# Kernel optimization log

Hardware: AMD Instinct MI355X
Metric: run time of the kernel (lower is better)

Reference implementation:

```python
import jax, jax.numpy as jnp
import numpy as np

N = 50000
E = 800000
D = 128
NCLASS = 10


def setup_inputs() -> dict:
    key = jax.random.key(0)
    ks = jax.random.split(key, 12)
    stdv = 1.0 / np.sqrt(D)
    inp = {
        "x": jax.random.normal(ks[0], (N, D), dtype=jnp.float32),
        "edge_src": jax.random.randint(ks[1], (E,), 0, N, dtype=jnp.int32),
        "edge_dst": jax.random.randint(ks[2], (E,), 0, N, dtype=jnp.int32),
        "edge_weight": jax.random.uniform(ks[3], (E,), dtype=jnp.float32),
        "W1": jax.random.uniform(ks[4], (D, D), jnp.float32, -stdv, stdv),
        "b1": jax.random.uniform(ks[5], (D,), jnp.float32, -stdv, stdv),
        "W2": jax.random.uniform(ks[6], (D, D), jnp.float32, -stdv, stdv),
        "b2": jax.random.uniform(ks[7], (D,), jnp.float32, -stdv, stdv),
        "W3": jax.random.uniform(ks[8], (D, D), jnp.float32, -stdv, stdv),
        "b3": jax.random.uniform(ks[9], (D,), jnp.float32, -stdv, stdv),
        "lin_W": jax.random.normal(ks[10], (NCLASS, 3 * D), dtype=jnp.float32) * 0.05,
        "lin_b": jax.random.normal(ks[11], (NCLASS,), dtype=jnp.float32) * 0.05,
    }
    return inp


def _gcn_layer(h, W, b, edge_src, edge_dst, edge_weight):
    # support = h @ W  (dense GEMM), then spmm(adj, support) as gather-scale-scatter
    support = h @ W                                   # [N, out]
    msgs = support[edge_src] * edge_weight[:, None]   # [E, out]
    agg = jax.ops.segment_sum(msgs, edge_dst, num_segments=h.shape[0])
    return agg + b


def reference(x, edge_src, edge_dst, edge_weight, W1, b1, W2, b2, W3, b3, lin_W, lin_b):
    x1 = jax.nn.relu(_gcn_layer(x, W1, b1, edge_src, edge_dst, edge_weight))
    o1 = jnp.max(x1, axis=0)
    x2 = jax.nn.relu(_gcn_layer(x1, W2, b2, edge_src, edge_dst, edge_weight))
    o2 = jnp.max(x2, axis=0)
    x3 = _gcn_layer(x2, W3, b3, edge_src, edge_dst, edge_weight)
    o3 = jnp.max(x3, axis=0)
    lin_in = jnp.concatenate([o1, o2, o3], axis=0)    # [3*D]
    logits = lin_W @ lin_in + lin_b                   # [nclass]
    return jax.nn.log_softmax(logits, axis=0)
```

## Files before the change

### kernel.cpp

```cpp
#include <hip/hip_runtime.h>
#include <hip/hip_bf16.h>
#include <math.h>

#define NN 50000
#define NPAD 50048
#define NE 800000
#define DD 128
#define NCLS 10
#define SCAN_BLOCK 1024
#define NTILES ((NN + 1 + SCAN_BLOCK - 1) / SCAN_BLOCK)

typedef short s16x8 __attribute__((ext_vector_type(8)));
typedef float f32x4 __attribute__((ext_vector_type(4)));

__device__ __forceinline__ unsigned short f2bf(float x) {
  __hip_bfloat16 h = __float2bfloat16(x);
  return __builtin_bit_cast(unsigned short, h);
}
__device__ __forceinline__ float bflo(unsigned int u) { return __uint_as_float(u << 16); }
__device__ __forceinline__ float bfhi(unsigned int u) { return __uint_as_float(u & 0xFFFF0000u); }

__device__ __forceinline__ unsigned int fkey(float f) {
  unsigned int u = __float_as_uint(f);
  return u ^ ((u & 0x80000000u) ? 0xFFFFFFFFu : 0x80000000u);
}
__device__ __forceinline__ float funkey(unsigned int k) {
  unsigned int u = (k & 0x80000000u) ? (k ^ 0x80000000u) : ~k;
  return __uint_as_float(u);
}

__global__ void k_count(const int* __restrict__ edst, int* __restrict__ offs) {
  int e = blockIdx.x * blockDim.x + threadIdx.x;
  if (e < NE) atomicAdd(&offs[edst[e] + 1], 1);
}

__global__ void k_scan_partial(const int* __restrict__ offs, int* __restrict__ bsum) {
  __shared__ int red[SCAN_BLOCK];
  int i = blockIdx.x * SCAN_BLOCK + threadIdx.x;
  red[threadIdx.x] = (i < NN + 1) ? offs[i] : 0;
  __syncthreads();
  for (int off = SCAN_BLOCK / 2; off > 0; off >>= 1) {
    if ((int)threadIdx.x < off) red[threadIdx.x] += red[threadIdx.x + off];
    __syncthreads();
  }
  if (threadIdx.x == 0) bsum[blockIdx.x] = red[0];
}

__global__ void k_scan_bsum(int* __restrict__ bsum) {
  if (threadIdx.x == 0) {
    int run = 0;
    for (int i = 0; i < NTILES; ++i) { int v = bsum[i]; bsum[i] = run; run += v; }
  }
}

__global__ void k_scan_final(int* __restrict__ offs, const int* __restrict__ bsum,
                             int* __restrict__ cursor) {
  __shared__ int tmp[SCAN_BLOCK];
  int i = blockIdx.x * SCAN_BLOCK + threadIdx.x;
  int v = (i < NN + 1) ? offs[i] : 0;
  tmp[threadIdx.x] = v;
  __syncthreads();
  for (int off = 1; off < SCAN_BLOCK; off <<= 1) {
    int t = ((int)threadIdx.x >= off) ? tmp[threadIdx.x - off] : 0;
    __syncthreads();
    tmp[threadIdx.x] += t;
    __syncthreads();
  }
  int incl = tmp[threadIdx.x] + bsum[blockIdx.x];
  if (i < NN + 1) {
    offs[i] = incl;
    if (i < NN) cursor[i] = incl;
  }
}

__global__ void k_fill(const int* __restrict__ esrc, const int* __restrict__ edst,
                       const float* __restrict__ ew, int* __restrict__ cursor,
                       int2* __restrict__ csr) {
  int e = blockIdx.x * blockDim.x + threadIdx.x;
  if (e < NE) {
    int d = edst[e];
    int p = atomicAdd(&cursor[d], 1);
    csr[p] = make_int2(esrc[e], __float_as_int(ew[e]));
  }
}

__global__ __launch_bounds__(256) void k_cvtW(const float* __restrict__ W1,
    const float* __restrict__ W2, const float* __restrict__ W3,
    unsigned short* __restrict__ WT1, unsigned short* __restrict__ WT2,
    unsigned short* __restrict__ WT3, unsigned int* __restrict__ omax) {
  int i = blockIdx.x * 256 + threadIdx.x;
  if (i < 3 * DD) omax[i] = 0u;
  if (i < DD * DD) {
    int k = i >> 7, c = i & 127;
    WT1[c * DD + k] = f2bf(W1[i]);
    WT2[c * DD + k] = f2bf(W2[i]);
    WT3[c * DD + k] = f2bf(W3[i]);
  }
}

template <int F32IN>
__global__ __launch_bounds__(256) void k_mm(const void* __restrict__ Hv,
                                            const unsigned short* __restrict__ Wt,
                                            unsigned short* __restrict__ S) {
  __shared__ unsigned short Hl[32 * DD];
  char* lb = (char*)Hl;
  const int wave = threadIdx.x >> 6, lane = threadIdx.x & 63;
  const int l15 = lane & 15, lk16 = (lane >> 4);
  const int r0 = blockIdx.x * 32;

#pragma unroll
  for (int j = 0; j < 2; ++j) {
    const int idx = threadIdx.x + j * 256;
    const int B = idx * 16;
    const int row = B >> 8;
    const int addr = B ^ ((row & 7) << 4);
    if (F32IN) {
      const float* H = (const float*)Hv;
      const int r = r0 + row;
      float4 a = make_float4(0.f, 0.f, 0.f, 0.f), b = a;
      if (r < NN) {
        const float* src = H + (size_t)r * DD + ((B & 255) >> 1);
        a = *(const float4*)src;
        b = *(const float4*)(src + 4);
      }
      uint4 pv;
      pv.x = (uint)f2bf(a.x) | ((uint)f2bf(a.y) << 16);
      pv.y = (uint)f2bf(a.z) | ((uint)f2bf(a.w) << 16);
      pv.z = (uint)f2bf(b.x) | ((uint)f2bf(b.y) << 16);
      pv.w = (uint)f2bf(b.z) | ((uint)f2bf(b.w) << 16);
      *(uint4*)(lb + addr) = pv;
    } else {
      const char* H = (const char*)Hv;
      uint4 v = *(const uint4*)(H + (size_t)r0 * 256 + B);
      *(uint4*)(lb + addr) = v;
    }
  }
  __syncthreads();

  const int cbase = wave * 32;
  s16x8 Af[2][4];
#pragma unroll
  for (int m = 0; m < 2; ++m)
#pragma unroll
    for (int ks = 0; ks < 4; ++ks)
      Af[m][ks] = *(const s16x8*)&Wt[(cbase + m * 16 + l15) * DD + ks * 32 + lk16 * 8];

  s16x8 Bf[2][4];
#pragma unroll
  for (int n = 0; n < 2; ++n) {
    const int row = n * 16 + l15;
#pragma unroll
    for (int ks = 0; ks < 4; ++ks) {
      const int B = row * 256 + ks * 64 + lk16 * 16;
      Bf[n][ks] = *(const s16x8*)(lb + (B ^ ((row & 7) << 4)));
    }
  }

  f32x4 acc[2][2];
#pragma unroll
  for (int m = 0; m < 2; ++m)
#pragma unroll
    for (int n = 0; n < 2; ++n) acc[m][n] = (f32x4){0.f, 0.f, 0.f, 0.f};

#pragma unroll
  for (int ks = 0; ks < 4; ++ks)
#pragma unroll
    for (int m = 0; m < 2; ++m)
#pragma unroll
      for (int n = 0; n < 2; ++n)
        acc[m][n] = __builtin_amdgcn_mfma_f32_16x16x32_bf16(Af[m][ks], Bf[n][ks],
                                                            acc[m][n], 0, 0, 0);

  __syncthreads();
#pragma unroll
  for (int m = 0; m < 2; ++m)
#pragma unroll
    for (int n = 0; n < 2; ++n) {
      const int row = n * 16 + l15;
      const int colb = (cbase + m * 16 + 4 * lk16) * 2;
      const int B = row * 256 + colb;
      uint2 pv;
      pv.x = (uint)f2bf(acc[m][n][0]) | ((uint)f2bf(acc[m][n][1]) << 16);
      pv.y = (uint)f2bf(acc[m][n][2]) | ((uint)f2bf(acc[m][n][3]) << 16);
      *(uint2*)(lb + (B ^ ((row & 7) << 4))) = pv;
    }
  __syncthreads();
#pragma unroll
  for (int j = 0; j < 2; ++j) {
    const int idx = threadIdx.x + j * 256;
    const int B = idx * 16;
    const int row = B >> 8;
    uint4 v = *(const uint4*)(lb + (B ^ ((row & 7) << 4)));
    *(uint4*)((char*)S + (size_t)r0 * 256 + B) = v;
  }
}

__device__ __forceinline__ void fma8(float* acc, float w, uint4 u) {
  acc[0] = fmaf(w, bflo(u.x), acc[0]);
  acc[1] = fmaf(w, bfhi(u.x), acc[1]);
  acc[2] = fmaf(w, bflo(u.y), acc[2]);
  acc[3] = fmaf(w, bfhi(u.y), acc[3]);
  acc[4] = fmaf(w, bflo(u.z), acc[4]);
  acc[5] = fmaf(w, bfhi(u.z), acc[5]);
  acc[6] = fmaf(w, bflo(u.w), acc[6]);
  acc[7] = fmaf(w, bfhi(u.w), acc[7]);
}

__global__ __launch_bounds__(256) void k_agg(const unsigned short* __restrict__ S,
                                             const int2* __restrict__ csr,
                                             const int* __restrict__ offs,
                                             const float* __restrict__ bias,
                                             unsigned short* __restrict__ Xout,
                                             unsigned int* __restrict__ omax,
                                             int do_relu) {
  __shared__ unsigned int cmax[DD];
  for (int i = threadIdx.x; i < DD; i += 256) cmax[i] = 0u;
  __syncthreads();
  const int lane = threadIdx.x & 63;
  const int wave = threadIdx.x >> 6;
  const int q = lane >> 4;
  const int t = lane & 15;
  const int gwave = blockIdx.x * 4 + wave;
  const int nwaves = gridDim.x * 4;
  const unsigned short* Scol = S + t * 8;

  float bcol[8];
  {
    float4 b0 = *(const float4*)&bias[t * 8];
    float4 b1 = *(const float4*)&bias[t * 8 + 4];
    bcol[0] = b0.x; bcol[1] = b0.y; bcol[2] = b0.z; bcol[3] = b0.w;
    bcol[4] = b1.x; bcol[5] = b1.y; bcol[6] = b1.z; bcol[7] = b1.w;
  }
  float mx[8];
#pragma unroll
  for (int j = 0; j < 8; ++j) mx[j] = -INFINITY;

  for (int d0 = gwave * 2; d0 < NN; d0 += nwaves * 2) {
    const int oA = offs[d0];
    const int oM = offs[d0 + 1];
    const int oE = offs[d0 + 2];
    int eA = oA + q; const int eA1 = oM;
    int eB = oM + q; const int eB1 = oE;
    float accA[8] = {0.f, 0.f, 0.f, 0.f, 0.f, 0.f, 0.f, 0.f};
    float accB[8] = {0.f, 0.f, 0.f, 0.f, 0.f, 0.f, 0.f, 0.f};

    while (__any((eA < eA1) || (eB < eB1))) {
      const bool pa0 = eA < eA1,      pa1 = eA + 4 < eA1;
      const bool pa2 = eA + 8 < eA1,  pa3 = eA + 12 < eA1;
      const bool pb0 = eB < eB1,      pb1 = eB + 4 < eB1;
      const bool pb2 = eB + 8 < eB1,  pb3 = eB + 12 < eB1;
      int2 a0, a1, a2, a3, b0, b1, b2, b3;
      if (pa0) a0 = csr[eA];
      if (pa1) a1 = csr[eA + 4];
      if (pa2) a2 = csr[eA + 8];
      if (pa3) a3 = csr[eA + 12];
      if (pb0) b0 = csr[eB];
      if (pb1) b1 = csr[eB + 4];
      if (pb2) b2 = csr[eB + 8];
      if (pb3) b3 = csr[eB + 12];
      uint4 uA0, uA1, uA2, uA3, uB0, uB1, uB2, uB3;
      if (pa0) uA0 = *(const uint4*)&Scol[(size_t)a0.x * DD];
      if (pa1) uA1 = *(const uint4*)&Scol[(size_t)a1.x * DD];
      if (pa2) uA2 = *(const uint4*)&Scol[(size_t)a2.x * DD];
      if (pa3) uA3 = *(const uint4*)&Scol[(size_t)a3.x * DD];
      if (pb0) uB0 = *(const uint4*)&Scol[(size_t)b0.x * DD];
      if (pb1) uB1 = *(const uint4*)&Scol[(size_t)b1.x * DD];
      if (pb2) uB2 = *(const uint4*)&Scol[(size_t)b2.x * DD];
      if (pb3) uB3 = *(const uint4*)&Scol[(size_t)b3.x * DD];
      if (pa0) fma8(accA, __int_as_float(a0.y), uA0);
      if (pa1) fma8(accA, __int_as_float(a1.y), uA1);
      if (pa2) fma8(accA, __int_as_float(a2.y), uA2);
      if (pa3) fma8(accA, __int_as_float(a3.y), uA3);
      if (pb0) fma8(accB, __int_as_float(b0.y), uB0);
      if (pb1) fma8(accB, __int_as_float(b1.y), uB1);
      if (pb2) fma8(accB, __int_as_float(b2.y), uB2);
      if (pb3) fma8(accB, __int_as_float(b3.y), uB3);
      eA += 16; eB += 16;
    }

#pragma unroll
    for (int j = 0; j < 8; ++j) {
      accA[j] += __shfl_xor(accA[j], 16, 64);
      accA[j] += __shfl_xor(accA[j], 32, 64);
      accA[j] += bcol[j];
      accB[j] += __shfl_xor(accB[j], 16, 64);
      accB[j] += __shfl_xor(accB[j], 32, 64);
      accB[j] += bcol[j];
      if (do_relu) {
        accA[j] = fmaxf(accA[j], 0.f);
        accB[j] = fmaxf(accB[j], 0.f);
      }
      mx[j] = fmaxf(mx[j], fmaxf(accA[j], accB[j]));
    }
    if (Xout) {
      if (q == 0) {
        uint4 xv;
        xv.x = (uint)f2bf(accA[0]) | ((uint)f2bf(accA[1]) << 16);
        xv.y = (uint)f2bf(accA[2]) | ((uint)f2bf(accA[3]) << 16);
        xv.z = (uint)f2bf(accA[4]) | ((uint)f2bf(accA[5]) << 16);
        xv.w = (uint)f2bf(accA[6]) | ((uint)f2bf(accA[7]) << 16);
        *(uint4*)&Xout[(size_t)d0 * DD + t * 8] = xv;
      } else if (q == 1) {
        uint4 xv;
        xv.x = (uint)f2bf(accB[0]) | ((uint)f2bf(accB[1]) << 16);
        xv.y = (uint)f2bf(accB[2]) | ((uint)f2bf(accB[3]) << 16);
        xv.z = (uint)f2bf(accB[4]) | ((uint)f2bf(accB[5]) << 16);
        xv.w = (uint)f2bf(accB[6]) | ((uint)f2bf(accB[7]) << 16);
        *(uint4*)&Xout[(size_t)(d0 + 1) * DD + t * 8] = xv;
      }
    }
  }
  if (q == 0) {
#pragma unroll
    for (int j = 0; j < 8; ++j) atomicMax(&cmax[t * 8 + j], fkey(mx[j]));
  }
  __syncthreads();
  for (int i = threadIdx.x; i < DD; i += 256) atomicMax(&omax[i], cmax[i]);
}

__global__ void k_head(const unsigned int* __restrict__ omax,
                       const float* __restrict__ linW,
                       const float* __restrict__ linb,
                       float* __restrict__ out) {
  __shared__ float o[3 * DD];
  __shared__ float logits[NCLS];
  int t = threadIdx.x;
  if (t < 3 * DD) o[t] = funkey(omax[t]);
  __syncthreads();
  if (t < NCLS) {
    float acc = linb[t];
    for (int j = 0; j < 3 * DD; ++j) acc = fmaf(linW[t * 3 * DD + j], o[j], acc);
    logits[t] = acc;
  }
  __syncthreads();
  if (t == 0) {
    float m = -INFINITY;
    for (int c = 0; c < NCLS; ++c) m = fmaxf(m, logits[c]);
    float s = 0.f;
    for (int c = 0; c < NCLS; ++c) s += expf(logits[c] - m);
    float ls = logf(s);
    for (int c = 0; c < NCLS; ++c) out[c] = logits[c] - m - ls;
  }
}

extern "C" void kernel_launch(void* const* d_in, const int* in_sizes, int n_in,
                              void* d_out, int out_size, void* d_ws, size_t ws_size,
                              hipStream_t stream) {
  const float* x    = (const float*)d_in[0];
  const int*   esrc = (const int*)d_in[1];
  const int*   edst = (const int*)d_in[2];
  const float* ew   = (const float*)d_in[3];
  const float* W1   = (const float*)d_in[4];
  const float* b1   = (const float*)d_in[5];
  const float* W2   = (const float*)d_in[6];
  const float* b2   = (const float*)d_in[7];
  const float* W3   = (const float*)d_in[8];
  const float* b3   = (const float*)d_in[9];
  const float* linW = (const float*)d_in[10];
  const float* linb = (const float*)d_in[11];
  float* out = (float*)d_out;

  size_t off = 0;
  auto alloc = [&](size_t bytes) {
    void* p = (char*)d_ws + off;
    off += (bytes + 255) & ~(size_t)255;
    return p;
  };
  unsigned short* X1   = (unsigned short*)alloc((size_t)NPAD * DD * 2);
  unsigned short* X2   = (unsigned short*)alloc((size_t)NPAD * DD * 2);
  unsigned short* S    = (unsigned short*)alloc((size_t)NPAD * DD * 2);
  unsigned short* WT1  = (unsigned short*)alloc((size_t)DD * DD * 2);
  unsigned short* WT2  = (unsigned short*)alloc((size_t)DD * DD * 2);
  unsigned short* WT3  = (unsigned short*)alloc((size_t)DD * DD * 2);
  int*          offs   = (int*)alloc((NN + 2) * 4);
  int*          cursor = (int*)alloc(NN * 4);
  int2*         csr    = (int2*)alloc((size_t)NE * 8);
  unsigned int* omax   = (unsigned int*)alloc(3 * DD * 4);
  int*          bsum   = (int*)alloc(NTILES * 4);
  (void)ws_size; (void)n_in; (void)in_sizes; (void)out_size;

  hipMemsetAsync(offs, 0, (NN + 2) * 4, stream);
  k_count<<<(NE + 255) / 256, 256, 0, stream>>>(edst, offs);
  k_scan_partial<<<NTILES, SCAN_BLOCK, 0, stream>>>(offs, bsum);
  k_scan_bsum<<<1, 64, 0, stream>>>(bsum);
  k_scan_final<<<NTILES, SCAN_BLOCK, 0, stream>>>(offs, bsum, cursor);
  k_fill<<<(NE + 255) / 256, 256, 0, stream>>>(esrc, edst, ew, cursor, csr);

  k_cvtW<<<(DD * DD + 255) / 256, 256, 0, stream>>>(W1, W2, W3, WT1, WT2, WT3, omax);

  const int mm_grid = NPAD / 32;
  k_mm<1><<<mm_grid, 256, 0, stream>>>(x, WT1, S);
  k_agg<<<2048, 256, 0, stream>>>(S, csr, offs, b1, X1, omax, 1);
  k_mm<0><<<mm_grid, 256, 0, stream>>>(X1, WT2, S);
  k_agg<<<2048, 256, 0, stream>>>(S, csr, offs, b2, X2, omax + DD, 1);
  k_mm<0><<<mm_grid, 256, 0, stream>>>(X2, WT3, S);
  k_agg<<<2048, 256, 0, stream>>>(S, csr, offs, b3, nullptr, omax + 2 * DD, 0);

  k_head<<<1, 384, 0, stream>>>(omax, linW, linb, out);
}
```

Measured before the change: 447.8 us.

## Split aggregation into column slices with XCD-aware block mapping and nontemporal loads

The aggregation kernel now gives each wave one destination node and only a 32-column slice of the feature row, instead of two nodes across all 128 columns. The slice is picked from blockIdx modulo 8, so blocks working on the same slice presumably land on the same XCD and share a smaller L2 working set. Each lane group now gathers 8 bytes per edge, and CSR reads and output writes use nontemporal hints. In exchange, the CSR edge list is read four times (once per slice), there are more gather instructions per byte, and the cross-lane reduction gains an extra shuffle stage.

New measurement: 461.4 us. +3.0%, slower.

```diff
diff --git a/kernel.cpp b/kernel.cpp
--- a/kernel.cpp
+++ b/kernel.cpp
@@ -195,127 +195,87 @@
   }
 }
 
-__device__ __forceinline__ void fma8(float* acc, float w, uint4 u) {
-  acc[0] = fmaf(w, bflo(u.x), acc[0]);
-  acc[1] = fmaf(w, bfhi(u.x), acc[1]);
-  acc[2] = fmaf(w, bflo(u.y), acc[2]);
-  acc[3] = fmaf(w, bfhi(u.y), acc[3]);
-  acc[4] = fmaf(w, bflo(u.z), acc[4]);
-  acc[5] = fmaf(w, bfhi(u.z), acc[5]);
-  acc[6] = fmaf(w, bflo(u.w), acc[6]);
-  acc[7] = fmaf(w, bfhi(u.w), acc[7]);
-}
-
 __global__ __launch_bounds__(256) void k_agg(const unsigned short* __restrict__ S,
-                                             const int2* __restrict__ csr,
+                                             const long* __restrict__ csr8,
                                              const int* __restrict__ offs,
                                              const float* __restrict__ bias,
                                              unsigned short* __restrict__ Xout,
                                              unsigned int* __restrict__ omax,
                                              int do_relu) {
-  __shared__ unsigned int cmax[DD];
-  for (int i = threadIdx.x; i < DD; i += 256) cmax[i] = 0u;
+  __shared__ unsigned int cmax[32];
+  if (threadIdx.x < 32) cmax[threadIdx.x] = 0u;
   __syncthreads();
   const int lane = threadIdx.x & 63;
   const int wave = threadIdx.x >> 6;
-  const int q = lane >> 4;
-  const int t = lane & 15;
-  const int gwave = blockIdx.x * 4 + wave;
-  const int nwaves = gridDim.x * 4;
-  const unsigned short* Scol = S + t * 8;
-
-  float bcol[8];
-  {
-    float4 b0 = *(const float4*)&bias[t * 8];
-    float4 b1 = *(const float4*)&bias[t * 8 + 4];
-    bcol[0] = b0.x; bcol[1] = b0.y; bcol[2] = b0.z; bcol[3] = b0.w;
-    bcol[4] = b1.x; bcol[5] = b1.y; bcol[6] = b1.z; bcol[7] = b1.w;
-  }
-  float mx[8];
-#pragma unroll
-  for (int j = 0; j < 8; ++j) mx[j] = -INFINITY;
-
-  for (int d0 = gwave * 2; d0 < NN; d0 += nwaves * 2) {
-    const int oA = offs[d0];
-    const int oM = offs[d0 + 1];
-    const int oE = offs[d0 + 2];
-    int eA = oA + q; const int eA1 = oM;
-    int eB = oM + q; const int eB1 = oE;
-    float accA[8] = {0.f, 0.f, 0.f, 0.f, 0.f, 0.f, 0.f, 0.f};
-    float accB[8] = {0.f, 0.f, 0.f, 0.f, 0.f, 0.f, 0.f, 0.f};
-
-    while (__any((eA < eA1) || (eB < eB1))) {
-      const bool pa0 = eA < eA1,      pa1 = eA + 4 < eA1;
-      const bool pa2 = eA + 8 < eA1,  pa3 = eA + 12 < eA1;
-      const bool pb0 = eB < eB1,      pb1 = eB + 4 < eB1;
-      const bool pb2 = eB + 8 < eB1,  pb3 = eB + 12 < eB1;
-      int2 a0, a1, a2, a3, b0, b1, b2, b3;
-      if (pa0) a0 = csr[eA];
-      if (pa1) a1 = csr[eA + 4];
-      if (pa2) a2 = csr[eA + 8];
-      if (pa3) a3 = csr[eA + 12];
-      if (pb0) b0 = csr[eB];
-      if (pb1) b1 = csr[eB + 4];
-      if (pb2) b2 = csr[eB + 8];
-      if (pb3) b3 = csr[eB + 12];
-      uint4 uA0, uA1, uA2, uA3, uB0, uB1, uB2, uB3;
-      if (pa0) uA0 = *(const uint4*)&Scol[(size_t)a0.x * DD];
-      if (pa1) uA1 = *(const uint4*)&Scol[(size_t)a1.x * DD];
-      if (pa2) uA2 = *(const uint4*)&Scol[(size_t)a2.x * DD];
-      if (pa3) uA3 = *(const uint4*)&Scol[(size_t)a3.x * DD];
-      if (pb0) uB0 = *(const uint4*)&Scol[(size_t)b0.x * DD];
-      if (pb1) uB1 = *(const uint4*)&Scol[(size_t)b1.x * DD];
-      if (pb2) uB2 = *(const uint4*)&Scol[(size_t)b2.x * DD];
-      if (pb3) uB3 = *(const uint4*)&Scol[(size_t)b3.x * DD];
-      if (pa0) fma8(accA, __int_as_float(a0.y), uA0);
-      if (pa1) fma8(accA, __int_as_float(a1.y), uA1);
-      if (pa2) fma8(accA, __int_as_float(a2.y), uA2);
-      if (pa3) fma8(accA, __int_as_float(a3.y), uA3);
-      if (pb0) fma8(accB, __int_as_float(b0.y), uB0);
-      if (pb1) fma8(accB, __int_as_float(b1.y), uB1);
-      if (pb2) fma8(accB, __int_as_float(b2.y), uB2);
-      if (pb3) fma8(accB, __int_as_float(b3.y), uB3);
-      eA += 16; eB += 16;
-    }
-
-#pragma unroll
-    for (int j = 0; j < 8; ++j) {
-      accA[j] += __shfl_xor(accA[j], 16, 64);
-      accA[j] += __shfl_xor(accA[j], 32, 64);
-      accA[j] += bcol[j];
-      accB[j] += __shfl_xor(accB[j], 16, 64);
-      accB[j] += __shfl_xor(accB[j], 32, 64);
-      accB[j] += bcol[j];
-      if (do_relu) {
-        accA[j] = fmaxf(accA[j], 0.f);
-        accB[j] = fmaxf(accB[j], 0.f);
+  const int g = lane >> 3;
+  const int t8 = lane & 7;
+  const int sgrp = blockIdx.x & 7;
+  const int slice = sgrp & 3;
+  const int half = sgrp >> 2;
+  const int bpg = (int)gridDim.x >> 3;
+  const int wsl = (half * bpg + (blockIdx.x >> 3)) * 4 + wave;
+  const int nstride = bpg * 8;
+  const int c0 = slice * 32 + t8 * 4;
+  const unsigned short* Sc = S + c0;
+
+  const float4 b4 = *(const float4*)&bias[c0];
+  float mx0 = -INFINITY, mx1 = -INFINITY, mx2 = -INFINITY, mx3 = -INFINITY;
+
+  for (int d = wsl; d < NN; d += nstride) {
+    const int e1 = offs[d + 1];
+    int e = offs[d] + g;
+    float a0 = 0.f, a1 = 0.f, a2 = 0.f, a3 = 0.f;
+    while (__any(e < e1)) {
+      const bool p0 = e < e1, p1 = e + 8 < e1;
+      long ce0 = 0, ce1 = 0;
+      if (p0) ce0 = __builtin_nontemporal_load(&csr8[e]);
+      if (p1) ce1 = __builtin_nontemporal_load(&csr8[e + 8]);
+      uint2 u0, u1;
+      if (p0) u0 = *(const uint2*)&Sc[(size_t)(int)ce0 * DD];
+      if (p1) u1 = *(const uint2*)&Sc[(size_t)(int)ce1 * DD];
+      if (p0) {
+        const float w = __uint_as_float((unsigned int)((unsigned long)ce0 >> 32));
+        a0 = fmaf(w, bflo(u0.x), a0);
+        a1 = fmaf(w, bfhi(u0.x), a1);
+        a2 = fmaf(w, bflo(u0.y), a2);
+        a3 = fmaf(w, bfhi(u0.y), a3);
       }
-      mx[j] = fmaxf(mx[j], fmaxf(accA[j], accB[j]));
-    }
-    if (Xout) {
-      if (q == 0) {
-        uint4 xv;
-        xv.x = (uint)f2bf(accA[0]) | ((uint)f2bf(accA[1]) << 16);
-        xv.y = (uint)f2bf(accA[2]) | ((uint)f2bf(accA[3]) << 16);
-        xv.z = (uint)f2bf(accA[4]) | ((uint)f2bf(accA[5]) << 16);
-        xv.w = (uint)f2bf(accA[6]) | ((uint)f2bf(accA[7]) << 16);
-        *(uint4*)&Xout[(size_t)d0 * DD + t * 8] = xv;
-      } else if (q == 1) {
-        uint4 xv;
-        xv.x = (uint)f2bf(accB[0]) | ((uint)f2bf(accB[1]) << 16);
-        xv.y = (uint)f2bf(accB[2]) | ((uint)f2bf(accB[3]) << 16);
-        xv.z = (uint)f2bf(accB[4]) | ((uint)f2bf(accB[5]) << 16);
-        xv.w = (uint)f2bf(accB[6]) | ((uint)f2bf(accB[7]) << 16);
-        *(uint4*)&Xout[(size_t)(d0 + 1) * DD + t * 8] = xv;
+      if (p1) {
+        const float w = __uint_as_float((unsigned int)((unsigned long)ce1 >> 32));
+        a0 = fmaf(w, bflo(u1.x), a0);
+        a1 = fmaf(w, bfhi(u1.x), a1);
+        a2 = fmaf(w, bflo(u1.y), a2);
+        a3 = fmaf(w, bfhi(u1.y), a3);
       }
-    }
-  }
-  if (q == 0) {
-#pragma unroll
-    for (int j = 0; j < 8; ++j) atomicMax(&cmax[t * 8 + j], fkey(mx[j]));
-  }
-  __syncthreads();
-  for (int i = threadIdx.x; i < DD; i += 256) atomicMax(&omax[i], cmax[i]);
+      e += 16;
+    }
+    a0 += __shfl_xor(a0, 8, 64);  a1 += __shfl_xor(a1, 8, 64);
+    a2 += __shfl_xor(a2, 8, 64);  a3 += __shfl_xor(a3, 8, 64);
+    a0 += __shfl_xor(a0, 16, 64); a1 += __shfl_xor(a1, 16, 64);
+    a2 += __shfl_xor(a2, 16, 64); a3 += __shfl_xor(a3, 16, 64);
+    a0 += __shfl_xor(a0, 32, 64); a1 += __shfl_xor(a1, 32, 64);
+    a2 += __shfl_xor(a2, 32, 64); a3 += __shfl_xor(a3, 32, 64);
+    a0 += b4.x; a1 += b4.y; a2 += b4.z; a3 += b4.w;
+    if (do_relu) {
+      a0 = fmaxf(a0, 0.f); a1 = fmaxf(a1, 0.f);
+      a2 = fmaxf(a2, 0.f); a3 = fmaxf(a3, 0.f);
+    }
+    mx0 = fmaxf(mx0, a0); mx1 = fmaxf(mx1, a1);
+    mx2 = fmaxf(mx2, a2); mx3 = fmaxf(mx3, a3);
+    if (Xout && g == 0) {
+      unsigned long lv = (unsigned long)((unsigned int)f2bf(a0) | ((unsigned int)f2bf(a1) << 16))
+                       | ((unsigned long)((unsigned int)f2bf(a2) | ((unsigned int)f2bf(a3) << 16)) << 32);
+      __builtin_nontemporal_store((long)lv, (long*)&Xout[(size_t)d * DD + c0]);
+    }
+  }
+  if (g == 0) {
+    atomicMax(&cmax[t8 * 4 + 0], fkey(mx0));
+    atomicMax(&cmax[t8 * 4 + 1], fkey(mx1));
+    atomicMax(&cmax[t8 * 4 + 2], fkey(mx2));
+    atomicMax(&cmax[t8 * 4 + 3], fkey(mx3));
+  }
+  __syncthreads();
+  if (threadIdx.x < 32) atomicMax(&omax[slice * 32 + threadIdx.x], cmax[threadIdx.x]);
 }
 
 __global__ void k_head(const unsigned int* __restrict__ omax,
@@ -389,12 +349,13 @@
   k_cvtW<<<(DD * DD + 255) / 256, 256, 0, stream>>>(W1, W2, W3, WT1, WT2, WT3, omax);
 
   const int mm_grid = NPAD / 32;
+  const long* csr8 = (const long*)csr;
   k_mm<1><<<mm_grid, 256, 0, stream>>>(x, WT1, S);
-  k_agg<<<2048, 256, 0, stream>>>(S, csr, offs, b1, X1, omax, 1);
+  k_agg<<<2048, 256, 0, stream>>>(S, csr8, offs, b1, X1, omax, 1);
   k_mm<0><<<mm_grid, 256, 0, stream>>>(X1, WT2, S);
-  k_agg<<<2048, 256, 0, stream>>>(S, csr, offs, b2, X2, omax + DD, 1);
+  k_agg<<<2048, 256, 0, stream>>>(S, csr8, offs, b2, X2, omax + DD, 1);
   k_mm<0><<<mm_grid, 256, 0, stream>>>(X2, WT3, S);
-  k_agg<<<2048, 256, 0, stream>>>(S, csr, offs, b3, nullptr, omax + 2 * DD, 0);
+  k_agg<<<2048, 256, 0, stream>>>(S, csr8, offs, b3, nullptr, omax + 2 * DD, 0);
 
   k_head<<<1, 384, 0, stream>>>(omax, linW, linb, out);
 }
```
